# Kernel optimization log

Hardware: AMD Instinct MI355X
Metric: run time of the kernel (lower is better)

## Reference

```python
import jax, jax.numpy as jnp
import numpy as np

B, C, H, W = 256, 32, 64, 64


def _affine_grid(theta, Hs, Ws):
    # theta: [B,2,3]; align_corners=False (PyTorch default). Returns [B,H,W,2] with (x,y) order.
    xs = (2.0 * jnp.arange(Ws, dtype=theta.dtype) + 1.0) / Ws - 1.0  # [W]
    ys = (2.0 * jnp.arange(Hs, dtype=theta.dtype) + 1.0) / Hs - 1.0  # [H]
    Xg, Yg = jnp.meshgrid(xs, ys)                                    # [H,W] each
    base = jnp.stack([Xg, Yg, jnp.ones_like(Xg)], axis=-1)           # [H,W,3]
    return jnp.einsum('bij,hwj->bhwi', theta, base)                  # [B,H,W,2]


def _grid_sample_bilinear(x, grid):
    # x: [B,C,H,W]; grid: [B,H,W,2] normalized (x,y); bilinear, zero padding, align_corners=False.
    Bs, Cs, Hs, Ws = x.shape
    gx = (grid[..., 0] + 1.0) * (Ws * 0.5) - 0.5
    gy = (grid[..., 1] + 1.0) * (Hs * 0.5) - 0.5
    x0 = jnp.floor(gx); y0 = jnp.floor(gy)
    x1 = x0 + 1.0;      y1 = y0 + 1.0
    wx1 = gx - x0; wx0 = 1.0 - wx1
    wy1 = gy - y0; wy0 = 1.0 - wy1

    def corner(xf, yf, w):
        valid = (xf >= 0) & (xf <= Ws - 1) & (yf >= 0) & (yf <= Hs - 1)
        xi = jnp.clip(xf, 0, Ws - 1).astype(jnp.int32)
        yi = jnp.clip(yf, 0, Hs - 1).astype(jnp.int32)
        vals = jax.vmap(lambda img, yy, xx: img[:, yy, xx])(x, yi, xi)  # [B,C,H,W] gather
        return vals * (w * valid)[:, None, :, :]

    return (corner(x0, y0, wx0 * wy0) + corner(x1, y0, wx1 * wy0)
            + corner(x0, y1, wx0 * wy1) + corner(x1, y1, wx1 * wy1))


def reference(x, w1, b1, w2, b2, w3, b3):
    Bs = x.shape[0]
    xs = x.reshape(Bs, -1)
    xs = jax.nn.relu(xs @ w1.T + b1)
    xs = jax.nn.relu(xs @ w2.T + b2)
    theta = (xs @ w3.T + b3).reshape(Bs, 2, 3)
    grid = _affine_grid(theta, x.shape[2], x.shape[3])
    return _grid_sample_bilinear(x, grid)


def setup_inputs() -> dict:
    key = jax.random.key(0)
    ks = jax.random.split(key, 8)
    fan1 = C * H * W
    x = jax.random.normal(ks[0], (B, C, H, W), dtype=jnp.float32)
    w1 = jax.random.normal(ks[1], (32, fan1), dtype=jnp.float32) / np.sqrt(fan1)
    b1 = jax.random.normal(ks[2], (32,), dtype=jnp.float32) * 0.01
    w2 = jax.random.normal(ks[3], (32, 32), dtype=jnp.float32) / np.sqrt(32.0)
    b2 = jax.random.normal(ks[4], (32,), dtype=jnp.float32) * 0.01
    w3 = jax.random.normal(ks[5], (6, 32), dtype=jnp.float32) * 0.001
    identity = jnp.array([1.0, 0.0, 0.0, 0.0, 1.0, 0.0], dtype=jnp.float32)
    b3 = identity + jax.random.normal(ks[6], (6,), dtype=jnp.float32) * 0.01
    return {"x": x, "w1": w1, "b1": b1, "w2": w2, "b2": b2, "w3": w3, "b3": b3}
```

## Files before the change

### kernel.cpp

```cpp
#include <hip/hip_runtime.h>
#include <hip/hip_bf16.h>


#define K_TOT 131072
#define KC    256
#define PKN   1024
#define STRB  ((size_t)PKN * 32)

typedef short s16x8 __attribute__((ext_vector_type(8)));
typedef float f32x4 __attribute__((ext_vector_type(4)));

struct __attribute__((aligned(4))) fpair { float a, b; };

__device__ __forceinline__ short f2bf(float f) {
    return __builtin_bit_cast(short, __float2bfloat16(f));
}
__device__ __forceinline__ float bf2f(short s) {
    const unsigned u = ((unsigned)(unsigned short)s) << 16;
    return __builtin_bit_cast(float, u);
}

__device__ __forceinline__ s16x8 cvt8(float4 a, float4 b) {
    s16x8 r;
    r[0] = f2bf(a.x); r[1] = f2bf(a.y); r[2] = f2bf(a.z); r[3] = f2bf(a.w);
    r[4] = f2bf(b.x); r[5] = f2bf(b.y); r[6] = f2bf(b.z); r[7] = f2bf(b.w);
    return r;
}

__device__ __forceinline__ void gload_lds16(const float* g, float* l) {
    __builtin_amdgcn_global_load_lds(
        (const __attribute__((address_space(1))) void*)(g),
        (__attribute__((address_space(3))) void*)(l),
        16, 0, 0);
}

__global__ __launch_bounds__(256) void st_p1k(const float* __restrict__ x,
                                              const float* __restrict__ w1,
                                              __hip_bfloat16* __restrict__ partial) {
    __shared__ __align__(16) float xbuf[2][16 * KC];

    const int bid  = blockIdx.x;
    const int t    = threadIdx.x;
    const int wv   = t >> 6;
    const int lane = t & 63;
    const int m    = lane & 15;
    const int kb   = lane >> 4;
    const int jh   = wv & 1;
    const int kh   = wv >> 1;

    const int xcd  = bid & 7;
    const int q    = bid >> 3;
    const int kc   = xcd * 64 + (q >> 1);
    const int half = q & 1;
    const size_t k0 = (size_t)kc * KC;

    const float* wq = w1 + (size_t)(jh * 16 + m) * K_TOT + k0 + (size_t)kh * 128 + kb * 8;
    float4 wr[8];
#pragma unroll
    for (int sss = 0; sss < 4; ++sss) {
        wr[2 * sss]     = *(const float4*)(wq + sss * 32);
        wr[2 * sss + 1] = *(const float4*)(wq + sss * 32 + 4);
    }

#pragma unroll
    for (int i2 = 0; i2 < 4; ++i2) {
        const int r = wv * 4 + i2;
        const int b0 = half * 128;
        const float* gsrc = x + (size_t)(b0 + r) * K_TOT + k0 + ((lane ^ (r & 7)) << 2);
        gload_lds16(gsrc, &xbuf[0][r * KC]);
    }

    s16x8 wf[4];
#pragma unroll
    for (int sss = 0; sss < 4; ++sss) wf[sss] = cvt8(wr[2 * sss], wr[2 * sss + 1]);

    const int pk = kc * 2 + kh;
    const int sw = m & 7;

#pragma unroll
    for (int it = 0; it < 8; ++it) {
        if (it + 1 < 8) {
            const int b0n = half * 128 + (it + 1) * 16;
#pragma unroll
            for (int i2 = 0; i2 < 4; ++i2) {
                const int r = wv * 4 + i2;
                const float* gsrc = x + (size_t)(b0n + r) * K_TOT + k0 + ((lane ^ (r & 7)) << 2);
                gload_lds16(gsrc, &xbuf[(it + 1) & 1][r * KC]);
            }
        }
        if (it == 0 || it == 7) asm volatile("s_waitcnt vmcnt(4)" ::: "memory");
        else                    asm volatile("s_waitcnt vmcnt(8)" ::: "memory");
        __builtin_amdgcn_s_barrier();
        __builtin_amdgcn_sched_barrier(0);

        const float* xr = &xbuf[it & 1][m * KC];
        f32x4 acc = {0.f, 0.f, 0.f, 0.f};
#pragma unroll
        for (int sss = 0; sss < 4; ++sss) {
            const int gb = kh * 32 + sss * 8 + kb * 2;
            const float4 fa = *(const float4*)(xr + ((gb ^ sw) << 2));
            const float4 fb = *(const float4*)(xr + (((gb + 1) ^ sw) << 2));
            const s16x8 af = cvt8(fa, fb);
            acc = __builtin_amdgcn_mfma_f32_16x16x32_bf16(af, wf[sss], acc, 0, 0, 0);
        }

        const int b0 = half * 128 + it * 16;
        __hip_bfloat16* p0 = partial + (size_t)(b0 + kb * 4) * STRB + (size_t)pk * 32 + jh * 16 + m;
#pragma unroll
        for (int rr = 0; rr < 4; ++rr)
            p0[(size_t)rr * STRB] = __float2bfloat16(acc[rr]);

        __builtin_amdgcn_s_barrier();
    }
}

__global__ __launch_bounds__(1024) void st_p2k(const __hip_bfloat16* __restrict__ partial,
                                               const float* __restrict__ b1,
                                               const float* __restrict__ w2,
                                               const float* __restrict__ b2,
                                               const float* __restrict__ w3,
                                               const float* __restrict__ b3,
                                               float* __restrict__ theta) {
    const int b = blockIdx.x;
    const int t = threadIdx.x;
    const s16x8* pb = (const s16x8*)(partial + (size_t)b * STRB);

    float a8[8] = {0.f, 0.f, 0.f, 0.f, 0.f, 0.f, 0.f, 0.f};
#pragma unroll
    for (int i = 0; i < 4; ++i) {
        const s16x8 u = pb[i * 1024 + t];
#pragma unroll
        for (int e = 0; e < 8; ++e) a8[e] += bf2f(u[e]);
    }

    __shared__ float red[1024][8];
    __shared__ float s1s[32];
    __shared__ float s2s[32];
#pragma unroll
    for (int e = 0; e < 8; ++e) red[t][e] = a8[e];
    __syncthreads();
#pragma unroll
    for (int off = 512; off >= 4; off >>= 1) {
        if (t < off) {
#pragma unroll
            for (int e = 0; e < 8; ++e) red[t][e] += red[t + off][e];
        }
        __syncthreads();
    }
    if (t < 4) {
#pragma unroll
        for (int e = 0; e < 8; ++e)
            s1s[8 * t + e] = fmaxf(red[t][e] + b1[8 * t + e], 0.f);
    }
    __syncthreads();
    if (t < 32) {
        float vv = b2[t];
#pragma unroll
        for (int i = 0; i < 32; ++i) vv += w2[t * 32 + i] * s1s[i];
        s2s[t] = fmaxf(vv, 0.f);
    }
    __syncthreads();
    if (t < 8) {
        float vv = 0.f;
        if (t < 6) {
            vv = b3[t];
#pragma unroll
            for (int i = 0; i < 32; ++i) vv += w3[t * 32 + i] * s2s[i];
        }
        theta[b * 8 + t] = vv;
    }
}

__global__ __launch_bounds__(256) void st_p3k(const float* __restrict__ x,
                                              const float* __restrict__ theta,
                                              float* __restrict__ out) {
    const int bid  = blockIdx.x;
    const int xcd  = bid & 7;
    const int s    = bid >> 3;
    const int b    = xcd * 32 + (s >> 4);
    const int sub  = s & 15;
    const int cgrp = sub >> 1;
    const int hh   = sub & 1;
    const int t    = threadIdx.x;
    const int w    = t & 63;
    const int hsub = t >> 6;

    const float* tb = theta + b * 8;
    const float t0 = tb[0], t1 = tb[1], t2 = tb[2];
    const float t3 = tb[3], t4 = tb[4], t5 = tb[5];

    const float* xb = x   + ((size_t)(b * 32 + cgrp * 4) << 12);
    float*       ob = out + ((size_t)(b * 32 + cgrp * 4) << 12);

    for (int hq = hh * 8; hq < hh * 8 + 8; ++hq) {
        const int h = hq * 4 + hsub;
        const float xs = ((float)w - 31.5f) * 0.03125f;
        const float ys = ((float)h - 31.5f) * 0.03125f;
        const float gxn = fmaf(t1, ys, fmaf(t0, xs, t2));
        const float gyn = fmaf(t4, ys, fmaf(t3, xs, t5));
        const float gx = fmaf(gxn, 32.f, 31.5f);
        const float gy = fmaf(gyn, 32.f, 31.5f);
        const float x0f = floorf(gx), y0f = floorf(gy);
        const float wx1 = gx - x0f, wx0 = 1.f - wx1;
        const float wy1 = gy - y0f, wy0 = 1.f - wy1;
        const int ix = (int)x0f, iy = (int)y0f;

        const float wx0v = wx0 * ((ix >= 0 && ix < 64) ? 1.f : 0.f);
        const float wx1v = wx1 * ((ix >= -1 && ix < 63) ? 1.f : 0.f);
        const int bx = min(max(ix, 0), 62);
        float wxa, wxb;
        if (ix == bx)     { wxa = wx0v; wxb = wx1v; }
        else if (ix < bx) { wxa = wx1v; wxb = 0.f; }
        else              { wxa = 0.f;  wxb = wx0v; }

        const float wy0v = wy0 * ((iy >= 0 && iy < 64) ? 1.f : 0.f);
        const float wy1v = wy1 * ((iy >= -1 && iy < 63) ? 1.f : 0.f);
        const int r0 = min(max(iy, 0), 63) * 64 + bx;
        const int r1 = min(max(iy + 1, 0), 63) * 64 + bx;

        const int off = h * 64 + w;
#pragma unroll
        for (int ci = 0; ci < 4; ++ci) {
            const float* img = xb + ((size_t)ci << 12);
            const fpair f0 = *(const fpair*)(img + r0);
            const fpair f1 = *(const fpair*)(img + r1);
            const float v = wy0v * (wxa * f0.a + wxb * f0.b)
                          + wy1v * (wxa * f1.a + wxb * f1.b);
            __builtin_nontemporal_store(v, ob + ((size_t)ci << 12) + off);
        }
    }
}

extern "C" void kernel_launch(void* const* d_in, const int* in_sizes, int n_in,
                              void* d_out, int out_size, void* d_ws, size_t ws_size,
                              hipStream_t stream) {
    const float* x  = (const float*)d_in[0];
    const float* w1 = (const float*)d_in[1];
    const float* b1 = (const float*)d_in[2];
    const float* w2 = (const float*)d_in[3];
    const float* b2 = (const float*)d_in[4];
    const float* w3 = (const float*)d_in[5];
    const float* b3 = (const float*)d_in[6];
    float* out = (float*)d_out;
    __hip_bfloat16* partial = (__hip_bfloat16*)d_ws;
    float* theta = (float*)(partial + (size_t)256 * STRB);

    st_p1k<<<1024, 256, 0, stream>>>(x, w1, partial);
    st_p2k<<<256, 1024, 0, stream>>>(partial, b1, w2, b2, w3, b3, theta);
    st_p3k<<<4096, 256, 0, stream>>>(x, theta, out);
}
```

Measured before the change: 77.62 us.

## Give each sampler thread a 2x4 pixel patch with row reuse and vector stores

The grid-sample kernel's thread mapping changes so each thread handles two adjacent columns across four consecutive rows instead of one pixel per row. When the next row's top source row matches the previous bottom row, the already-loaded pair is reused, which cuts gather loads. Output is written as 8-byte float2 nontemporal stores. The cost is more registers per thread and a data-dependent branch for the reuse check.

```diff
diff --git a/kernel.cpp b/kernel.cpp
--- a/kernel.cpp
+++ b/kernel.cpp
@@ -9,6 +9,7 @@
 
 typedef short s16x8 __attribute__((ext_vector_type(8)));
 typedef float f32x4 __attribute__((ext_vector_type(4)));
+typedef float f32x2 __attribute__((ext_vector_type(2)));
 
 struct __attribute__((aligned(4))) fpair { float a, b; };
 
@@ -182,8 +183,8 @@
     const int cgrp = sub >> 1;
     const int hh   = sub & 1;
     const int t    = threadIdx.x;
-    const int w    = t & 63;
-    const int hsub = t >> 6;
+    const int wp   = t & 31;
+    const int hsub = t >> 5;
 
     const float* tb = theta + b * 8;
     const float t0 = tb[0], t1 = tb[1], t2 = tb[2];
@@ -192,41 +193,65 @@
     const float* xb = x   + ((size_t)(b * 32 + cgrp * 4) << 12);
     float*       ob = out + ((size_t)(b * 32 + cgrp * 4) << 12);
 
-    for (int hq = hh * 8; hq < hh * 8 + 8; ++hq) {
-        const int h = hq * 4 + hsub;
-        const float xs = ((float)w - 31.5f) * 0.03125f;
+    const int h0 = hh * 32 + hsub * 4;
+
+    int   prevR1[2];
+    fpair pf1[2][4];
+
+#pragma unroll
+    for (int i = 0; i < 4; ++i) {
+        const int h = h0 + i;
         const float ys = ((float)h - 31.5f) * 0.03125f;
-        const float gxn = fmaf(t1, ys, fmaf(t0, xs, t2));
-        const float gyn = fmaf(t4, ys, fmaf(t3, xs, t5));
-        const float gx = fmaf(gxn, 32.f, 31.5f);
-        const float gy = fmaf(gyn, 32.f, 31.5f);
-        const float x0f = floorf(gx), y0f = floorf(gy);
-        const float wx1 = gx - x0f, wx0 = 1.f - wx1;
-        const float wy1 = gy - y0f, wy0 = 1.f - wy1;
-        const int ix = (int)x0f, iy = (int)y0f;
-
-        const float wx0v = wx0 * ((ix >= 0 && ix < 64) ? 1.f : 0.f);
-        const float wx1v = wx1 * ((ix >= -1 && ix < 63) ? 1.f : 0.f);
-        const int bx = min(max(ix, 0), 62);
-        float wxa, wxb;
-        if (ix == bx)     { wxa = wx0v; wxb = wx1v; }
-        else if (ix < bx) { wxa = wx1v; wxb = 0.f; }
-        else              { wxa = 0.f;  wxb = wx0v; }
-
-        const float wy0v = wy0 * ((iy >= 0 && iy < 64) ? 1.f : 0.f);
-        const float wy1v = wy1 * ((iy >= -1 && iy < 63) ? 1.f : 0.f);
-        const int r0 = min(max(iy, 0), 63) * 64 + bx;
-        const int r1 = min(max(iy + 1, 0), 63) * 64 + bx;
-
-        const int off = h * 64 + w;
+        float val[2][4];
+
+#pragma unroll
+        for (int wi = 0; wi < 2; ++wi) {
+            const int w = 2 * wp + wi;
+            const float xs = ((float)w - 31.5f) * 0.03125f;
+            const float gxn = fmaf(t1, ys, fmaf(t0, xs, t2));
+            const float gyn = fmaf(t4, ys, fmaf(t3, xs, t5));
+            const float gx = fmaf(gxn, 32.f, 31.5f);
+            const float gy = fmaf(gyn, 32.f, 31.5f);
+            const float x0f = floorf(gx), y0f = floorf(gy);
+            const float wx1 = gx - x0f, wx0 = 1.f - wx1;
+            const float wy1 = gy - y0f, wy0 = 1.f - wy1;
+            const int ix = (int)x0f, iy = (int)y0f;
+
+            const float wx0v = wx0 * ((ix >= 0 && ix < 64) ? 1.f : 0.f);
+            const float wx1v = wx1 * ((ix >= -1 && ix < 63) ? 1.f : 0.f);
+            const int bx = min(max(ix, 0), 62);
+            float wxa, wxb;
+            if (ix == bx)     { wxa = wx0v; wxb = wx1v; }
+            else if (ix < bx) { wxa = wx1v; wxb = 0.f; }
+            else              { wxa = 0.f;  wxb = wx0v; }
+
+            const float wy0v = wy0 * ((iy >= 0 && iy < 64) ? 1.f : 0.f);
+            const float wy1v = wy1 * ((iy >= -1 && iy < 63) ? 1.f : 0.f);
+            const int r0 = min(max(iy, 0), 63) * 64 + bx;
+            const int r1 = min(max(iy + 1, 0), 63) * 64 + bx;
+
+            const bool reuse = (i > 0) && (r0 == prevR1[wi]);
+#pragma unroll
+            for (int ci = 0; ci < 4; ++ci) {
+                const float* pl = xb + ((size_t)ci << 12);
+                fpair f0;
+                if (reuse) f0 = pf1[wi][ci];
+                else       f0 = *(const fpair*)(pl + r0);
+                const fpair f1 = *(const fpair*)(pl + r1);
+                pf1[wi][ci] = f1;
+                val[wi][ci] = wy0v * (wxa * f0.a + wxb * f0.b)
+                            + wy1v * (wxa * f1.a + wxb * f1.b);
+            }
+            prevR1[wi] = r1;
+        }
+
+        const int off = h * 64 + 2 * wp;
 #pragma unroll
         for (int ci = 0; ci < 4; ++ci) {
-            const float* img = xb + ((size_t)ci << 12);
-            const fpair f0 = *(const fpair*)(img + r0);
-            const fpair f1 = *(const fpair*)(img + r1);
-            const float v = wy0v * (wxa * f0.a + wxb * f0.b)
-                          + wy1v * (wxa * f1.a + wxb * f1.b);
-            __builtin_nontemporal_store(v, ob + ((size_t)ci << 12) + off);
+            f32x2 v2;
+            v2.x = val[0][ci];
+            v2.y = val[1][ci];
+            __builtin_nontemporal_store(v2, (f32x2*)(ob + ((size_t)ci << 12) + off));
         }
     }
 }
```

New measurement: 81.11 us. 1.04x slower.
